# Kernel tuning notes

Measured on AMD Instinct MI355X. Metric: run time of the kernel, lower is better.

Reference implementation:

```python
import jax, jax.numpy as jnp
import numpy as np

U, SI, TI = 100000, 50000, 40000
D = 64
B = 8192
NNZ_S, NNZ_T = 3_200_000, 2_560_000
P_DROP = 0.2


def setup_inputs() -> dict:
    key = jax.random.key(0)
    ks = iter(jax.random.split(key, 32))
    nxt = lambda: next(ks)
    emb = lambda n: (jax.random.normal(nxt(), (n, D), jnp.float32) * 0.1)
    keep = lambda n: jax.random.bernoulli(nxt(), 1.0 - P_DROP, (n,)).astype(jnp.float32) / (1.0 - P_DROP)
    inp = {}
    inp['user'] = jax.random.randint(nxt(), (B,), 0, U, jnp.int32)
    inp['source_pos_item'] = jax.random.randint(nxt(), (B,), 0, SI, jnp.int32)
    inp['source_neg_item'] = jax.random.randint(nxt(), (B,), 0, SI, jnp.int32)
    inp['target_pos_item'] = jax.random.randint(nxt(), (B,), 0, TI, jnp.int32)
    inp['target_neg_item'] = jax.random.randint(nxt(), (B,), 0, TI, jnp.int32)
    inp['mask_s'] = jax.random.bernoulli(nxt(), 0.5, (B,))
    inp['mask_t'] = jax.random.bernoulli(nxt(), 0.5, (B,))
    inp['su_int'] = emb(U); inp['si_int'] = emb(SI)
    inp['tu_int'] = emb(U); inp['ti_int'] = emb(TI)
    inp['su_pop'] = emb(U); inp['si_pop'] = emb(SI)
    inp['tu_pop'] = emb(U); inp['ti_pop'] = emb(TI)
    Ns, Nt = U + SI, U + TI
    inp['s_rows'] = jax.random.randint(nxt(), (NNZ_S,), 0, Ns, jnp.int32)
    inp['s_cols'] = jax.random.randint(nxt(), (NNZ_S,), 0, Ns, jnp.int32)
    inp['s_vals'] = jax.random.uniform(nxt(), (NNZ_S,), jnp.float32, 0.0, 0.02)
    inp['t_rows'] = jax.random.randint(nxt(), (NNZ_T,), 0, Nt, jnp.int32)
    inp['t_cols'] = jax.random.randint(nxt(), (NNZ_T,), 0, Nt, jnp.int32)
    inp['t_vals'] = jax.random.uniform(nxt(), (NNZ_T,), jnp.float32, 0.0, 0.02)
    inp['drop_s_int'] = keep(NNZ_S); inp['drop_t_int'] = keep(NNZ_T)
    inp['drop_s_pop'] = keep(NNZ_S); inp['drop_t_pop'] = keep(NNZ_T)
    return inp


def _lightgcn(emb, rows, cols, vals, n_users):
    # 1-layer LightGCN: out = mean([e0, A @ e0]) ; A given as COO (rows, cols, vals)
    agg = jax.ops.segment_sum(vals[:, None] * emb[cols], rows, num_segments=emb.shape[0])
    out = 0.5 * (emb + agg)
    return out[:n_users], out[n_users:]


def _bpr(p, n):
    return -jnp.mean(jax.nn.log_sigmoid(p - n))


def _mask_bpr(p, n, m):
    return -jnp.mean(m.astype(p.dtype) * jax.nn.log_sigmoid(p - n))


def _masked_l1(a, b, idx):
    # L1Loss(mean) over rows selected by unique(idx); membership mask avoids jnp.unique
    m = jnp.zeros((a.shape[0],), bool).at[idx].set(True)
    cnt = jnp.maximum(m.sum(), 1).astype(a.dtype)
    return jnp.sum(jnp.abs(a - b) * m[:, None]) / (cnt * a.shape[1])


def reference(user, source_pos_item, source_neg_item, target_pos_item, target_neg_item,
              mask_s, mask_t,
              su_int, si_int, tu_int, ti_int, su_pop, si_pop, tu_pop, ti_pop,
              s_rows, s_cols, s_vals, t_rows, t_cols, t_vals,
              drop_s_int, drop_t_int, drop_s_pop, drop_t_pop):
    # int factor
    us_i, is_i = _lightgcn(jnp.concatenate([su_int, si_int]), s_rows, s_cols, s_vals * drop_s_int, U)
    ut_i, it_i = _lightgcn(jnp.concatenate([tu_int, ti_int]), t_rows, t_cols, t_vals * drop_t_int, U)
    # pop factor
    us_p, is_p = _lightgcn(jnp.concatenate([su_pop, si_pop]), s_rows, s_cols, s_vals * drop_s_pop, U)
    ut_p, it_p = _lightgcn(jnp.concatenate([tu_pop, ti_pop]), t_rows, t_cols, t_vals * drop_t_pop, U)

    dot = lambda ue, ie, u, i: jnp.sum(ue[u] * ie[i], axis=1)
    sp_i = dot(us_i, is_i, user, source_pos_item); sn_i = dot(us_i, is_i, user, source_neg_item)
    sp_p = dot(us_p, is_p, user, source_pos_item); sn_p = dot(us_p, is_p, user, source_neg_item)
    tp_i = dot(ut_i, it_i, user, target_pos_item); tn_i = dot(ut_i, it_i, user, target_neg_item)
    tp_p = dot(ut_p, it_p, user, target_pos_item); tn_p = dot(ut_p, it_p, user, target_neg_item)

    loss_int_s = _mask_bpr(sp_i, sn_i, mask_s)
    loss_pop_s = _mask_bpr(sn_p, sp_p, mask_s) + _mask_bpr(sp_p, sn_p, ~mask_s)
    loss_int_t = _mask_bpr(tp_i, tn_i, mask_t)
    loss_pop_t = _mask_bpr(tn_p, tp_p, mask_t) + _mask_bpr(tp_p, tn_p, ~mask_t)
    loss_total_s = _bpr(sp_i + sp_p, sn_i + sn_p)
    loss_total_t = _bpr(tp_i + tp_p, tn_i + tn_p)

    item_all_s = jnp.concatenate([source_pos_item, source_neg_item])
    item_all_t = jnp.concatenate([target_pos_item, target_neg_item])
    dis_loss = (_masked_l1(su_int, su_pop, user) + _masked_l1(si_int, si_pop, item_all_s)
                + _masked_l1(tu_int, tu_pop, user) + _masked_l1(ti_int, ti_pop, item_all_t))

    loss = (loss_total_s + loss_total_t
            + 0.1 * (loss_int_s + loss_int_t)
            + 0.1 * (loss_pop_s + loss_pop_t)
            - 0.01 * dis_loss)
    return loss
```

## Files before the change

kernel.cpp:

```cpp
#include <hip/hip_runtime.h>
#include <math.h>

constexpr int U_N = 100000;
constexpr int SI_N = 50000;
constexpr int TI_N = 40000;
constexpr int D = 64;
constexpr int B = 8192;
constexpr int NS = U_N + SI_N;
constexpr int NT = U_N + TI_N;
constexpr int SLOTS = 3 * B;
constexpr int CAP = 48;
constexpr int OVCAP = 4096;
constexpr int NROWS_ALL = U_N + SI_N + TI_N;
constexpr int NCHUNK = (NROWS_ALL + 63) / 64;
constexpr int DOTS_BLOCKS = B / 4;
constexpr int L1_BLOCKS = 768;

__device__ __forceinline__ float wave_sum(float x) {
#pragma unroll
  for (int m = 32; m; m >>= 1) x += __shfl_xor(x, m, 64);
  return x;
}

__device__ __forceinline__ float softplus_f(float z) {
  return fmaxf(z, 0.f) + log1pf(expf(-fabsf(z)));
}

__global__ __launch_bounds__(256) void k_init(
    const int* __restrict__ user, const int* __restrict__ spos, const int* __restrict__ sneg,
    const int* __restrict__ tpos, const int* __restrict__ tneg,
    int* __restrict__ map_s, int* __restrict__ map_t,
    const unsigned char* __restrict__ m, int* __restrict__ det) {
  if (blockIdx.x < 96) {
    int t = blockIdx.x * blockDim.x + threadIdx.x;
    if (t < B) {
      int u = user[t];
      map_s[u] = t;
      map_t[u] = t;
    } else if (t < 2 * B) {
      int b = t - B;
      map_s[U_N + spos[b]] = t;
      map_t[U_N + tpos[b]] = t;
    } else {
      int b = t - 2 * B;
      map_s[U_N + sneg[b]] = t;
      map_t[U_N + tneg[b]] = t;
    }
    return;
  }
  int t = threadIdx.x;
  int cb = 0, cc = 0;
  for (int i = t; i < B; i += 256) {
    unsigned char v = m[i];
    if ((i & 3) && v) cb++;
    if (v > 1) cc++;
  }
#pragma unroll
  for (int off = 32; off; off >>= 1) {
    cb += __shfl_xor(cb, off, 64);
    cc += __shfl_xor(cc, off, 64);
  }
  __shared__ int sb[4], sc[4];
  if ((t & 63) == 0) { sb[t >> 6] = cb; sc[t >> 6] = cc; }
  __syncthreads();
  if (t == 0) {
    det[0] = sb[0] + sb[1] + sb[2] + sb[3];
    det[1] = sc[0] + sc[1] + sc[2] + sc[3];
  }
}

__device__ __forceinline__ void emit_edge(
    int slot, unsigned packed, float vp,
    int* __restrict__ cnt, int2* __restrict__ bucket,
    int* __restrict__ ovcnt, int4* __restrict__ ov) {
  int pos = atomicAdd(&cnt[slot], 1);
  if (pos < CAP) {
    bucket[(size_t)slot * CAP + pos] = make_int2((int)packed, __float_as_int(vp));
  } else {
    int o = atomicAdd(ovcnt, 1);
    if (o < OVCAP) {
      ov[o] = make_int4(slot, (int)packed, __float_as_int(vp), 0);
    }
  }
}

__global__ __launch_bounds__(256) void k_compact4(
    const int* __restrict__ s_rows, const int* __restrict__ s_cols,
    const float* __restrict__ s_vals,
    const float* __restrict__ dsi, const float* __restrict__ dsp,
    const int* __restrict__ t_rows, const int* __restrict__ t_cols,
    const float* __restrict__ t_vals,
    const float* __restrict__ dti, const float* __restrict__ dtp,
    const int* __restrict__ map_s, const int* __restrict__ map_t,
    int* __restrict__ cnt_s, int* __restrict__ cnt_t,
    int2* __restrict__ bucket_s, int2* __restrict__ bucket_t,
    int* __restrict__ ovcnt_s, int* __restrict__ ovcnt_t,
    int4* __restrict__ ov_s, int4* __restrict__ ov_t,
    int nnz_s, int nnz_t, int sblocks) {
  const int* rows;
  const int* cols;
  const float* vals;
  const float* di;
  const float* dp;
  const int* map;
  int* cnt;
  int2* bucket;
  int* ovcnt;
  int4* ov;
  int nnz;
  int blk = blockIdx.x;
  if (blk < sblocks) {
    rows = s_rows; cols = s_cols; vals = s_vals; di = dsi; dp = dsp;
    map = map_s; cnt = cnt_s; bucket = bucket_s; ovcnt = ovcnt_s; ov = ov_s;
    nnz = nnz_s;
  } else {
    blk -= sblocks;
    rows = t_rows; cols = t_cols; vals = t_vals; di = dti; dp = dtp;
    map = map_t; cnt = cnt_t; bucket = bucket_t; ovcnt = ovcnt_t; ov = ov_t;
    nnz = nnz_t;
  }
  int base = (blk * 256 + (int)threadIdx.x) * 4;
  if (base + 4 <= nnz) {
    int4 r4 = *(const int4*)(rows + base);
    int4 c4 = *(const int4*)(cols + base);
    float4 v4 = *(const float4*)(vals + base);
    float4 di4 = *(const float4*)(di + base);
    float4 dp4 = *(const float4*)(dp + base);
    int s0 = map[r4.x];
    int s1 = map[r4.y];
    int s2 = map[r4.z];
    int s3 = map[r4.w];
    unsigned b0 = (di4.x != 0.f ? 0x40000000u : 0u) | (dp4.x != 0.f ? 0x80000000u : 0u);
    unsigned b1 = (di4.y != 0.f ? 0x40000000u : 0u) | (dp4.y != 0.f ? 0x80000000u : 0u);
    unsigned b2 = (di4.z != 0.f ? 0x40000000u : 0u) | (dp4.z != 0.f ? 0x80000000u : 0u);
    unsigned b3 = (di4.w != 0.f ? 0x40000000u : 0u) | (dp4.w != 0.f ? 0x80000000u : 0u);
    if (s0 >= 0 && b0) emit_edge(s0, (unsigned)c4.x | b0, v4.x * fmaxf(di4.x, dp4.x), cnt, bucket, ovcnt, ov);
    if (s1 >= 0 && b1) emit_edge(s1, (unsigned)c4.y | b1, v4.y * fmaxf(di4.y, dp4.y), cnt, bucket, ovcnt, ov);
    if (s2 >= 0 && b2) emit_edge(s2, (unsigned)c4.z | b2, v4.z * fmaxf(di4.z, dp4.z), cnt, bucket, ovcnt, ov);
    if (s3 >= 0 && b3) emit_edge(s3, (unsigned)c4.w | b3, v4.w * fmaxf(di4.w, dp4.w), cnt, bucket, ovcnt, ov);
  } else {
    for (int e = base; e < nnz; ++e) {
      int slot = map[rows[e]];
      if (slot < 0) continue;
      unsigned bb = (di[e] != 0.f ? 0x40000000u : 0u) | (dp[e] != 0.f ? 0x80000000u : 0u);
      if (!bb) continue;
      emit_edge(slot, (unsigned)cols[e] | bb, vals[e] * fmaxf(di[e], dp[e]), cnt, bucket, ovcnt, ov);
    }
  }
}

__device__ __forceinline__ void accum_slot(
    int s, int lane,
    const int* __restrict__ cnt, const int2* __restrict__ bucket,
    const int* __restrict__ ovcnt, const int4* __restrict__ ov,
    const float* __restrict__ eu_i, const float* __restrict__ ei_i,
    const float* __restrict__ eu_p, const float* __restrict__ ei_p,
    float* __restrict__ aggA, float* __restrict__ aggB) {
  int li = min(lane, CAP - 1);
  int2 pl = bucket[(size_t)s * CAP + li];
  int m = min(cnt[s], CAP);
  int g = lane >> 4, sub = lane & 15;
  int c = 0;
  float wi = 0.f, wp = 0.f;
  if (lane < m) {
    unsigned packed = (unsigned)pl.x;
    float vp = __int_as_float(pl.y);
    c = (int)(packed & 0x3FFFFFFFu);
    wi = (packed & 0x40000000u) ? vp : 0.f;
    wp = (packed & 0x80000000u) ? vp : 0.f;
  }
  float aIx = 0, aIy = 0, aIz = 0, aIw = 0;
  float aPx = 0, aPy = 0, aPz = 0, aPw = 0;
  for (int k = 0; k < m; k += 16) {
    int i0 = k + g, i1 = k + 4 + g, i2 = k + 8 + g, i3 = k + 12 + g;
    int c0 = __shfl(c, i0, 64), c1 = __shfl(c, i1, 64);
    int c2 = __shfl(c, i2, 64), c3 = __shfl(c, i3, 64);
    float wi0 = __shfl(wi, i0, 64), wi1 = __shfl(wi, i1, 64);
    float wi2 = __shfl(wi, i2, 64), wi3 = __shfl(wi, i3, 64);
    float wp0 = __shfl(wp, i0, 64), wp1 = __shfl(wp, i1, 64);
    float wp2 = __shfl(wp, i2, 64), wp3 = __shfl(wp, i3, 64);
    const float* bi0 = (c0 < U_N) ? (eu_i + (size_t)c0 * D) : (ei_i + (size_t)(c0 - U_N) * D);
    const float* bi1 = (c1 < U_N) ? (eu_i + (size_t)c1 * D) : (ei_i + (size_t)(c1 - U_N) * D);
    const float* bi2 = (c2 < U_N) ? (eu_i + (size_t)c2 * D) : (ei_i + (size_t)(c2 - U_N) * D);
    const float* bi3 = (c3 < U_N) ? (eu_i + (size_t)c3 * D) : (ei_i + (size_t)(c3 - U_N) * D);
    const float* bp0 = (c0 < U_N) ? (eu_p + (size_t)c0 * D) : (ei_p + (size_t)(c0 - U_N) * D);
    const float* bp1 = (c1 < U_N) ? (eu_p + (size_t)c1 * D) : (ei_p + (size_t)(c1 - U_N) * D);
    const float* bp2 = (c2 < U_N) ? (eu_p + (size_t)c2 * D) : (ei_p + (size_t)(c2 - U_N) * D);
    const float* bp3 = (c3 < U_N) ? (eu_p + (size_t)c3 * D) : (ei_p + (size_t)(c3 - U_N) * D);
    float4 vI0 = *(const float4*)(bi0 + 4 * sub);
    float4 vI1 = *(const float4*)(bi1 + 4 * sub);
    float4 vI2 = *(const float4*)(bi2 + 4 * sub);
    float4 vI3 = *(const float4*)(bi3 + 4 * sub);
    float4 vP0 = *(const float4*)(bp0 + 4 * sub);
    float4 vP1 = *(const float4*)(bp1 + 4 * sub);
    float4 vP2 = *(const float4*)(bp2 + 4 * sub);
    float4 vP3 = *(const float4*)(bp3 + 4 * sub);
    aIx = fmaf(wi0, vI0.x, aIx); aIy = fmaf(wi0, vI0.y, aIy);
    aIz = fmaf(wi0, vI0.z, aIz); aIw = fmaf(wi0, vI0.w, aIw);
    aIx = fmaf(wi1, vI1.x, aIx); aIy = fmaf(wi1, vI1.y, aIy);
    aIz = fmaf(wi1, vI1.z, aIz); aIw = fmaf(wi1, vI1.w, aIw);
    aIx = fmaf(wi2, vI2.x, aIx); aIy = fmaf(wi2, vI2.y, aIy);
    aIz = fmaf(wi2, vI2.z, aIz); aIw = fmaf(wi2, vI2.w, aIw);
    aIx = fmaf(wi3, vI3.x, aIx); aIy = fmaf(wi3, vI3.y, aIy);
    aIz = fmaf(wi3, vI3.z, aIz); aIw = fmaf(wi3, vI3.w, aIw);
    aPx = fmaf(wp0, vP0.x, aPx); aPy = fmaf(wp0, vP0.y, aPy);
    aPz = fmaf(wp0, vP0.z, aPz); aPw = fmaf(wp0, vP0.w, aPw);
    aPx = fmaf(wp1, vP1.x, aPx); aPy = fmaf(wp1, vP1.y, aPy);
    aPz = fmaf(wp1, vP1.z, aPz); aPw = fmaf(wp1, vP1.w, aPw);
    aPx = fmaf(wp2, vP2.x, aPx); aPy = fmaf(wp2, vP2.y, aPy);
    aPz = fmaf(wp2, vP2.z, aPz); aPw = fmaf(wp2, vP2.w, aPw);
    aPx = fmaf(wp3, vP3.x, aPx); aPy = fmaf(wp3, vP3.y, aPy);
    aPz = fmaf(wp3, vP3.z, aPz); aPw = fmaf(wp3, vP3.w, aPw);
  }
#define XRED(x) x += __shfl_xor(x, 16, 64); x += __shfl_xor(x, 32, 64);
  XRED(aIx) XRED(aIy) XRED(aIz) XRED(aIw)
  XRED(aPx) XRED(aPy) XRED(aPz) XRED(aPw)
#undef XRED
  int nov = min(*ovcnt, OVCAP);
  for (int i = 0; i < nov; ++i) {
    int4 q = ov[i];
    if (q.x == s) {
      unsigned packed = (unsigned)q.y;
      float vp = __int_as_float(q.z);
      int cc = (int)(packed & 0x3FFFFFFFu);
      float wwi = (packed & 0x40000000u) ? vp : 0.f;
      float wwp = (packed & 0x80000000u) ? vp : 0.f;
      const float* bi = (cc < U_N) ? (eu_i + (size_t)cc * D) : (ei_i + (size_t)(cc - U_N) * D);
      const float* bp = (cc < U_N) ? (eu_p + (size_t)cc * D) : (ei_p + (size_t)(cc - U_N) * D);
      if (lane < 16) {
        float4 vI = *(const float4*)(bi + 4 * sub);
        float4 vP = *(const float4*)(bp + 4 * sub);
        aIx = fmaf(wwi, vI.x, aIx); aIy = fmaf(wwi, vI.y, aIy);
        aIz = fmaf(wwi, vI.z, aIz); aIw = fmaf(wwi, vI.w, aIw);
        aPx = fmaf(wwp, vP.x, aPx); aPy = fmaf(wwp, vP.y, aPy);
        aPz = fmaf(wwp, vP.z, aPz); aPw = fmaf(wwp, vP.w, aPw);
      }
    }
  }
  if (lane < 16) {
    *(float4*)(aggA + (size_t)s * D + 4 * sub) = make_float4(aIx, aIy, aIz, aIw);
    *(float4*)(aggB + (size_t)s * D + 4 * sub) = make_float4(aPx, aPy, aPz, aPw);
  }
}

__global__ __launch_bounds__(256) void k_accum_pair(
    const int* __restrict__ cnt_s, const int2* __restrict__ bucket_s,
    const int* __restrict__ ovcnt_s, const int4* __restrict__ ov_s,
    const int* __restrict__ cnt_t, const int2* __restrict__ bucket_t,
    const int* __restrict__ ovcnt_t, const int4* __restrict__ ov_t,
    const float* __restrict__ su_i, const float* __restrict__ si_i,
    const float* __restrict__ su_p, const float* __restrict__ si_p,
    const float* __restrict__ tu_i, const float* __restrict__ ti_i,
    const float* __restrict__ tu_p, const float* __restrict__ ti_p,
    float* __restrict__ aggSA, float* __restrict__ aggSB,
    float* __restrict__ aggTA, float* __restrict__ aggTB) {
  int lane = threadIdx.x & 63;
  int sg = (blockIdx.x * 256 + threadIdx.x) >> 6;
  if (sg >= 2 * SLOTS) return;
  if (sg < SLOTS) {
    accum_slot(sg, lane, cnt_s, bucket_s, ovcnt_s, ov_s,
               su_i, si_i, su_p, si_p, aggSA, aggSB);
  } else {
    accum_slot(sg - SLOTS, lane, cnt_t, bucket_t, ovcnt_t, ov_t,
               tu_i, ti_i, tu_p, ti_p, aggTA, aggTB);
  }
}

__global__ __launch_bounds__(256) void k_tail(
    const int* __restrict__ user,
    const int* __restrict__ spos, const int* __restrict__ sneg,
    const int* __restrict__ tpos, const int* __restrict__ tneg,
    const unsigned char* __restrict__ ms8, const unsigned char* __restrict__ mt8,
    const int* __restrict__ det,
    const float* __restrict__ su_i, const float* __restrict__ si_i,
    const float* __restrict__ su_p, const float* __restrict__ si_p,
    const float* __restrict__ tu_i, const float* __restrict__ ti_i,
    const float* __restrict__ tu_p, const float* __restrict__ ti_p,
    const int* __restrict__ map_s, const int* __restrict__ map_t,
    const float* __restrict__ aggSA, const float* __restrict__ aggSB,
    const float* __restrict__ aggTA, const float* __restrict__ aggTB,
    float* __restrict__ dots_part, float* __restrict__ l1_part) {
  int lane = threadIdx.x & 63;
  if (blockIdx.x < DOTS_BLOCKS) {
    int b = (blockIdx.x * blockDim.x + threadIdx.x) >> 6;
    float contrib = 0.f;
    {
      int u = user[b];
      int ps = spos[b], ns = sneg[b], pt = tpos[b], nt = tneg[b];
      int sus = map_s[u], sps = map_s[U_N + ps], sns = map_s[U_N + ns];
      int sut = map_t[u], spt = map_t[U_N + pt], snt = map_t[U_N + nt];
      float oui = su_i[(size_t)u * D + lane] + aggSA[(size_t)sus * D + lane];
      float oup = su_p[(size_t)u * D + lane] + aggSB[(size_t)sus * D + lane];
      float opi = si_i[(size_t)ps * D + lane] + aggSA[(size_t)sps * D + lane];
      float opp = si_p[(size_t)ps * D + lane] + aggSB[(size_t)sps * D + lane];
      float oni = si_i[(size_t)ns * D + lane] + aggSA[(size_t)sns * D + lane];
      float onp = si_p[(size_t)ns * D + lane] + aggSB[(size_t)sns * D + lane];
      float spi = 0.25f * wave_sum(oui * opi);
      float sni = 0.25f * wave_sum(oui * oni);
      float spp = 0.25f * wave_sum(oup * opp);
      float snp = 0.25f * wave_sum(oup * onp);
      float tui = tu_i[(size_t)u * D + lane] + aggTA[(size_t)sut * D + lane];
      float tup = tu_p[(size_t)u * D + lane] + aggTB[(size_t)sut * D + lane];
      float tpi_ = ti_i[(size_t)pt * D + lane] + aggTA[(size_t)spt * D + lane];
      float tpp_ = ti_p[(size_t)pt * D + lane] + aggTB[(size_t)spt * D + lane];
      float tni_ = ti_i[(size_t)nt * D + lane] + aggTA[(size_t)snt * D + lane];
      float tnp_ = ti_p[(size_t)nt * D + lane] + aggTB[(size_t)snt * D + lane];
      float tpi = 0.25f * wave_sum(tui * tpi_);
      float tni = 0.25f * wave_sum(tui * tni_);
      float tpp = 0.25f * wave_sum(tup * tpp_);
      float tnp = 0.25f * wave_sum(tup * tnp_);
      int db = det[0], dc = det[1];
      float ms, mt;
      if (dc > 100) {
        ms = (((const float*)ms8)[b] != 0.f) ? 1.f : 0.f;
        mt = (((const float*)mt8)[b] != 0.f) ? 1.f : 0.f;
      } else if (db > 100) {
        ms = ms8[b] ? 1.f : 0.f;
        mt = mt8[b] ? 1.f : 0.f;
      } else {
        ms = ((const int*)ms8)[b] ? 1.f : 0.f;
        mt = ((const int*)mt8)[b] ? 1.f : 0.f;
      }
      float l_int_s = ms * softplus_f(sni - spi);
      float l_pop_s = ms * softplus_f(spp - snp) + (1.f - ms) * softplus_f(snp - spp);
      float l_tot_s = softplus_f((sni + snp) - (spi + spp));
      float l_int_t = mt * softplus_f(tni - tpi);
      float l_pop_t = mt * softplus_f(tpp - tnp) + (1.f - mt) * softplus_f(tnp - tpp);
      float l_tot_t = softplus_f((tni + tnp) - (tpi + tpp));
      contrib = (l_tot_s + l_tot_t + 0.1f * (l_int_s + l_int_t) +
                 0.1f * (l_pop_s + l_pop_t)) * (1.f / (float)B);
    }
    __shared__ float wsum_[4];
    if (lane == 0) wsum_[threadIdx.x >> 6] = contrib;
    __syncthreads();
    if (threadIdx.x == 0) {
      dots_part[blockIdx.x] = wsum_[0] + wsum_[1] + wsum_[2] + wsum_[3];
    }
    return;
  }
  int blk = blockIdx.x - DOTS_BLOCKS;
  int wave = (blk * blockDim.x + threadIdx.x) >> 6;
  int nwaves = (L1_BLOCKS * 256) >> 6;
  float a1 = 0.f, a2 = 0.f, a3 = 0.f, a4 = 0.f;
  float c5 = 0.f, c6 = 0.f, c7 = 0.f;
  for (int ch = wave; ch < NCHUNK; ch += nwaves) {
    int r0 = ch * 64;
    int r = r0 + lane;
    int flag = -1;
    if (r < NROWS_ALL) flag = (r < NS) ? map_s[r] : map_t[r - SI_N];
    bool valid = flag >= 0;
    unsigned long long m0 = __ballot(valid && r < U_N);
    unsigned long long m1 = __ballot(valid && r >= U_N && r < NS);
    unsigned long long m2 = __ballot(valid && r >= NS);
    if (lane == 0) {
      c5 += (float)__popcll(m0);
      c6 += (float)__popcll(m1);
      c7 += (float)__popcll(m2);
    }
    unsigned long long mm = m0 | m1 | m2;
    while (mm) {
      int bit = __ffsll((unsigned long long)mm) - 1;
      mm &= mm - 1;
      int rr = r0 + bit;
      if (rr < U_N) {
        size_t o = (size_t)rr * D + lane;
        a1 += fabsf(su_i[o] - su_p[o]);
        a3 += fabsf(tu_i[o] - tu_p[o]);
      } else if (rr < NS) {
        size_t o = (size_t)(rr - U_N) * D + lane;
        a2 += fabsf(si_i[o] - si_p[o]);
      } else {
        size_t o = (size_t)(rr - NS) * D + lane;
        a4 += fabsf(ti_i[o] - ti_p[o]);
      }
    }
  }
  a1 = wave_sum(a1);
  a2 = wave_sum(a2);
  a3 = wave_sum(a3);
  a4 = wave_sum(a4);
  __shared__ float sb[4][8];
  if (lane == 0) {
    int w = threadIdx.x >> 6;
    sb[w][0] = a1; sb[w][1] = a2; sb[w][2] = a3; sb[w][3] = a4;
    sb[w][4] = c5; sb[w][5] = c6; sb[w][6] = c7;
  }
  __syncthreads();
  int t = threadIdx.x;
  if (t < 7) {
    l1_part[t * L1_BLOCKS + blk] = sb[0][t] + sb[1][t] + sb[2][t] + sb[3][t];
  }
}

__global__ __launch_bounds__(256) void k_finish(
    const float* __restrict__ dots_part, const float* __restrict__ l1_part,
    float* __restrict__ out) {
  int t = threadIdx.x, lane = t & 63, w = t >> 6;
  float a0 = 0.f;
  for (int i = t; i < DOTS_BLOCKS; i += 256) a0 += dots_part[i];
  float q[7];
#pragma unroll
  for (int j = 0; j < 7; ++j) {
    float s = 0.f;
    for (int i = t; i < L1_BLOCKS; i += 256) s += l1_part[j * L1_BLOCKS + i];
    q[j] = s;
  }
  a0 = wave_sum(a0);
#pragma unroll
  for (int j = 0; j < 7; ++j) q[j] = wave_sum(q[j]);
  __shared__ float red[4][8];
  if (lane == 0) {
    red[w][0] = a0;
#pragma unroll
    for (int j = 0; j < 7; ++j) red[w][1 + j] = q[j];
  }
  __syncthreads();
  if (t == 0) {
    float v[8];
#pragma unroll
    for (int j = 0; j < 8; ++j)
      v[j] = red[0][j] + red[1][j] + red[2][j] + red[3][j];
    float n1 = v[1], n2 = v[2], n3 = v[3], n4 = v[4];
    float cu = fmaxf(v[5], 1.f);
    float cs = fmaxf(v[6], 1.f);
    float ct = fmaxf(v[7], 1.f);
    float dis = (n1 + n3) / (cu * (float)D) + n2 / (cs * (float)D) +
                n4 / (ct * (float)D);
    out[0] = v[0] - 0.01f * dis;
  }
}

extern "C" void kernel_launch(void* const* d_in, const int* in_sizes, int n_in,
                              void* d_out, int out_size, void* d_ws, size_t ws_size,
                              hipStream_t stream) {
  const int* user = (const int*)d_in[0];
  const int* spos = (const int*)d_in[1];
  const int* sneg = (const int*)d_in[2];
  const int* tpos = (const int*)d_in[3];
  const int* tneg = (const int*)d_in[4];
  const unsigned char* mask_s = (const unsigned char*)d_in[5];
  const unsigned char* mask_t = (const unsigned char*)d_in[6];
  const float* su_int = (const float*)d_in[7];
  const float* si_int = (const float*)d_in[8];
  const float* tu_int = (const float*)d_in[9];
  const float* ti_int = (const float*)d_in[10];
  const float* su_pop = (const float*)d_in[11];
  const float* si_pop = (const float*)d_in[12];
  const float* tu_pop = (const float*)d_in[13];
  const float* ti_pop = (const float*)d_in[14];
  const int* s_rows = (const int*)d_in[15];
  const int* s_cols = (const int*)d_in[16];
  const float* s_vals = (const float*)d_in[17];
  const int* t_rows = (const int*)d_in[18];
  const int* t_cols = (const int*)d_in[19];
  const float* t_vals = (const float*)d_in[20];
  const float* drop_s_int = (const float*)d_in[21];
  const float* drop_t_int = (const float*)d_in[22];
  const float* drop_s_pop = (const float*)d_in[23];
  const float* drop_t_pop = (const float*)d_in[24];
  const int nnz_s = in_sizes[15];
  const int nnz_t = in_sizes[18];

  int4* ov_s = (int4*)d_ws;
  int4* ov_t = ov_s + OVCAP;
  int2* bucket_s = (int2*)(ov_t + OVCAP);
  int2* bucket_t = bucket_s + (size_t)SLOTS * CAP;
  float* aggSA = (float*)(bucket_t + (size_t)SLOTS * CAP);
  float* aggSB = aggSA + (size_t)SLOTS * D;
  float* aggTA = aggSB + (size_t)SLOTS * D;
  float* aggTB = aggTA + (size_t)SLOTS * D;
  float* dots_part = aggTB + (size_t)SLOTS * D;
  float* l1_part = dots_part + DOTS_BLOCKS;
  int* det = (int*)(l1_part + 7 * L1_BLOCKS);
  int* ovcnt_s = det + 2;
  int* ovcnt_t = ovcnt_s + 1;
  int* cnt_s = ovcnt_t + 1;
  int* cnt_t = cnt_s + SLOTS;
  int* map_s = cnt_t + SLOTS;
  int* map_t = map_s + NS;

  hipMemsetAsync(det, 0, (size_t)(2 + 2 + 2 * SLOTS) * sizeof(int), stream);
  hipMemsetAsync(map_s, 0xFF, (size_t)(NS + NT) * sizeof(int), stream);

  k_init<<<97, 256, 0, stream>>>(user, spos, sneg, tpos, tneg, map_s, map_t, mask_s, det);

  int sblocks = (nnz_s + 1023) / 1024;
  int tblocks = (nnz_t + 1023) / 1024;
  k_compact4<<<sblocks + tblocks, 256, 0, stream>>>(
      s_rows, s_cols, s_vals, drop_s_int, drop_s_pop,
      t_rows, t_cols, t_vals, drop_t_int, drop_t_pop,
      map_s, map_t, cnt_s, cnt_t, bucket_s, bucket_t,
      ovcnt_s, ovcnt_t, ov_s, ov_t, nnz_s, nnz_t, sblocks);

  k_accum_pair<<<2 * SLOTS / 4, 256, 0, stream>>>(
      cnt_s, bucket_s, ovcnt_s, ov_s, cnt_t, bucket_t, ovcnt_t, ov_t,
      su_int, si_int, su_pop, si_pop, tu_int, ti_int, tu_pop, ti_pop,
      aggSA, aggSB, aggTA, aggTB);

  k_tail<<<DOTS_BLOCKS + L1_BLOCKS, 256, 0, stream>>>(
      user, spos, sneg, tpos, tneg, mask_s, mask_t, det,
      su_int, si_int, su_pop, si_pop, tu_int, ti_int, tu_pop, ti_pop,
      map_s, map_t, aggSA, aggSB, aggTA, aggTB,
      dots_part, l1_part);

  k_finish<<<1, 256, 0, stream>>>(dots_part, l1_part, (float*)d_out);
}
```

Baseline: 400.5 us.

## Partition edge bucket counters per XCD to avoid cross-die atomic contention

Edge compaction now writes into eight separate per-XCD bucket and counter arrays, selected by blockIdx modulo 8, each holding 12 entries per slot. The idea is that atomics on each counter stay within one die's L2 instead of bouncing across XCDs. The accumulate step reads all eight counters per slot, forms prefix offsets, and gathers entries from the matching partition. This adds more counter reads, a more complex gather, and a larger memset. Overflow risk rises because each partition holds only 12 entries, so skew past that falls into the shared linear overflow scan.

```diff
diff --git a/kernel.cpp b/kernel.cpp
--- a/kernel.cpp
+++ b/kernel.cpp
@@ -9,7 +9,8 @@
 constexpr int NS = U_N + SI_N;
 constexpr int NT = U_N + TI_N;
 constexpr int SLOTS = 3 * B;
-constexpr int CAP = 48;
+constexpr int NXCD = 8;
+constexpr int CAP_X = 12;
 constexpr int OVCAP = 4096;
 constexpr int NROWS_ALL = U_N + SI_N + TI_N;
 constexpr int NCHUNK = (NROWS_ALL + 63) / 64;
@@ -74,8 +75,8 @@
     int* __restrict__ cnt, int2* __restrict__ bucket,
     int* __restrict__ ovcnt, int4* __restrict__ ov) {
   int pos = atomicAdd(&cnt[slot], 1);
-  if (pos < CAP) {
-    bucket[(size_t)slot * CAP + pos] = make_int2((int)packed, __float_as_int(vp));
+  if (pos < CAP_X) {
+    bucket[(size_t)slot * CAP_X + pos] = make_int2((int)packed, __float_as_int(vp));
   } else {
     int o = atomicAdd(ovcnt, 1);
     if (o < OVCAP) {
@@ -119,6 +120,9 @@
     map = map_t; cnt = cnt_t; bucket = bucket_t; ovcnt = ovcnt_t; ov = ov_t;
     nnz = nnz_t;
   }
+  int p = (int)(blockIdx.x & (NXCD - 1));
+  cnt += (size_t)p * SLOTS;
+  bucket += (size_t)p * SLOTS * CAP_X;
   int base = (blk * 256 + (int)threadIdx.x) * 4;
   if (base + 4 <= nnz) {
     int4 r4 = *(const int4*)(rows + base);
@@ -156,61 +160,80 @@
     const float* __restrict__ eu_i, const float* __restrict__ ei_i,
     const float* __restrict__ eu_p, const float* __restrict__ ei_p,
     float* __restrict__ aggA, float* __restrict__ aggB) {
-  int li = min(lane, CAP - 1);
-  int2 pl = bucket[(size_t)s * CAP + li];
-  int m = min(cnt[s], CAP);
+  int c0 = min(cnt[0 * SLOTS + s], CAP_X);
+  int c1 = min(cnt[1 * SLOTS + s], CAP_X);
+  int c2 = min(cnt[2 * SLOTS + s], CAP_X);
+  int c3 = min(cnt[3 * SLOTS + s], CAP_X);
+  int c4 = min(cnt[4 * SLOTS + s], CAP_X);
+  int c5 = min(cnt[5 * SLOTS + s], CAP_X);
+  int c6 = min(cnt[6 * SLOTS + s], CAP_X);
+  int c7 = min(cnt[7 * SLOTS + s], CAP_X);
+  int p1 = c0, p2 = p1 + c1, p3 = p2 + c2, p4 = p3 + c3;
+  int p5 = p4 + c4, p6 = p5 + c5, p7 = p6 + c6;
+  int m = p7 + c7;
   int g = lane >> 4, sub = lane & 15;
-  int c = 0;
-  float wi = 0.f, wp = 0.f;
-  if (lane < m) {
-    unsigned packed = (unsigned)pl.x;
-    float vp = __int_as_float(pl.y);
-    c = (int)(packed & 0x3FFFFFFFu);
-    wi = (packed & 0x40000000u) ? vp : 0.f;
-    wp = (packed & 0x80000000u) ? vp : 0.f;
-  }
   float aIx = 0, aIy = 0, aIz = 0, aIw = 0;
   float aPx = 0, aPy = 0, aPz = 0, aPw = 0;
-  for (int k = 0; k < m; k += 16) {
-    int i0 = k + g, i1 = k + 4 + g, i2 = k + 8 + g, i3 = k + 12 + g;
-    int c0 = __shfl(c, i0, 64), c1 = __shfl(c, i1, 64);
-    int c2 = __shfl(c, i2, 64), c3 = __shfl(c, i3, 64);
-    float wi0 = __shfl(wi, i0, 64), wi1 = __shfl(wi, i1, 64);
-    float wi2 = __shfl(wi, i2, 64), wi3 = __shfl(wi, i3, 64);
-    float wp0 = __shfl(wp, i0, 64), wp1 = __shfl(wp, i1, 64);
-    float wp2 = __shfl(wp, i2, 64), wp3 = __shfl(wp, i3, 64);
-    const float* bi0 = (c0 < U_N) ? (eu_i + (size_t)c0 * D) : (ei_i + (size_t)(c0 - U_N) * D);
-    const float* bi1 = (c1 < U_N) ? (eu_i + (size_t)c1 * D) : (ei_i + (size_t)(c1 - U_N) * D);
-    const float* bi2 = (c2 < U_N) ? (eu_i + (size_t)c2 * D) : (ei_i + (size_t)(c2 - U_N) * D);
-    const float* bi3 = (c3 < U_N) ? (eu_i + (size_t)c3 * D) : (ei_i + (size_t)(c3 - U_N) * D);
-    const float* bp0 = (c0 < U_N) ? (eu_p + (size_t)c0 * D) : (ei_p + (size_t)(c0 - U_N) * D);
-    const float* bp1 = (c1 < U_N) ? (eu_p + (size_t)c1 * D) : (ei_p + (size_t)(c1 - U_N) * D);
-    const float* bp2 = (c2 < U_N) ? (eu_p + (size_t)c2 * D) : (ei_p + (size_t)(c2 - U_N) * D);
-    const float* bp3 = (c3 < U_N) ? (eu_p + (size_t)c3 * D) : (ei_p + (size_t)(c3 - U_N) * D);
-    float4 vI0 = *(const float4*)(bi0 + 4 * sub);
-    float4 vI1 = *(const float4*)(bi1 + 4 * sub);
-    float4 vI2 = *(const float4*)(bi2 + 4 * sub);
-    float4 vI3 = *(const float4*)(bi3 + 4 * sub);
-    float4 vP0 = *(const float4*)(bp0 + 4 * sub);
-    float4 vP1 = *(const float4*)(bp1 + 4 * sub);
-    float4 vP2 = *(const float4*)(bp2 + 4 * sub);
-    float4 vP3 = *(const float4*)(bp3 + 4 * sub);
-    aIx = fmaf(wi0, vI0.x, aIx); aIy = fmaf(wi0, vI0.y, aIy);
-    aIz = fmaf(wi0, vI0.z, aIz); aIw = fmaf(wi0, vI0.w, aIw);
-    aIx = fmaf(wi1, vI1.x, aIx); aIy = fmaf(wi1, vI1.y, aIy);
-    aIz = fmaf(wi1, vI1.z, aIz); aIw = fmaf(wi1, vI1.w, aIw);
-    aIx = fmaf(wi2, vI2.x, aIx); aIy = fmaf(wi2, vI2.y, aIy);
-    aIz = fmaf(wi2, vI2.z, aIz); aIw = fmaf(wi2, vI2.w, aIw);
-    aIx = fmaf(wi3, vI3.x, aIx); aIy = fmaf(wi3, vI3.y, aIy);
-    aIz = fmaf(wi3, vI3.z, aIz); aIw = fmaf(wi3, vI3.w, aIw);
-    aPx = fmaf(wp0, vP0.x, aPx); aPy = fmaf(wp0, vP0.y, aPy);
-    aPz = fmaf(wp0, vP0.z, aPz); aPw = fmaf(wp0, vP0.w, aPw);
-    aPx = fmaf(wp1, vP1.x, aPx); aPy = fmaf(wp1, vP1.y, aPy);
-    aPz = fmaf(wp1, vP1.z, aPz); aPw = fmaf(wp1, vP1.w, aPw);
-    aPx = fmaf(wp2, vP2.x, aPx); aPy = fmaf(wp2, vP2.y, aPy);
-    aPz = fmaf(wp2, vP2.z, aPz); aPw = fmaf(wp2, vP2.w, aPw);
-    aPx = fmaf(wp3, vP3.x, aPx); aPy = fmaf(wp3, vP3.y, aPy);
-    aPz = fmaf(wp3, vP3.z, aPz); aPw = fmaf(wp3, vP3.w, aPw);
+  for (int bb = 0; bb < m; bb += 64) {
+    int l = bb + lane;
+    int c = 0;
+    float wi = 0.f, wp = 0.f;
+    if (l < m) {
+      int x = (l >= p1) + (l >= p2) + (l >= p3) + (l >= p4) +
+              (l >= p5) + (l >= p6) + (l >= p7);
+      int pre = (x >= 1 ? c0 : 0) + (x >= 2 ? c1 : 0) + (x >= 3 ? c2 : 0) +
+                (x >= 4 ? c3 : 0) + (x >= 5 ? c4 : 0) + (x >= 6 ? c5 : 0) +
+                (x >= 7 ? c6 : 0);
+      int j = l - pre;
+      int2 pl = bucket[((size_t)x * SLOTS + s) * CAP_X + j];
+      unsigned packed = (unsigned)pl.x;
+      float vp = __int_as_float(pl.y);
+      c = (int)(packed & 0x3FFFFFFFu);
+      wi = (packed & 0x40000000u) ? vp : 0.f;
+      wp = (packed & 0x80000000u) ? vp : 0.f;
+    }
+    int mb = min(m - bb, 64);
+    for (int k = 0; k < mb; k += 16) {
+      int i0 = k + g, i1 = k + 4 + g, i2 = k + 8 + g, i3 = k + 12 + g;
+      int cc0 = __shfl(c, i0, 64), cc1 = __shfl(c, i1, 64);
+      int cc2 = __shfl(c, i2, 64), cc3 = __shfl(c, i3, 64);
+      float wi0 = __shfl(wi, i0, 64), wi1 = __shfl(wi, i1, 64);
+      float wi2 = __shfl(wi, i2, 64), wi3 = __shfl(wi, i3, 64);
+      float wp0 = __shfl(wp, i0, 64), wp1 = __shfl(wp, i1, 64);
+      float wp2 = __shfl(wp, i2, 64), wp3 = __shfl(wp, i3, 64);
+      const float* bi0 = (cc0 < U_N) ? (eu_i + (size_t)cc0 * D) : (ei_i + (size_t)(cc0 - U_N) * D);
+      const float* bi1 = (cc1 < U_N) ? (eu_i + (size_t)cc1 * D) : (ei_i + (size_t)(cc1 - U_N) * D);
+      const float* bi2 = (cc2 < U_N) ? (eu_i + (size_t)cc2 * D) : (ei_i + (size_t)(cc2 - U_N) * D);
+      const float* bi3 = (cc3 < U_N) ? (eu_i + (size_t)cc3 * D) : (ei_i + (size_t)(cc3 - U_N) * D);
+      const float* bp0 = (cc0 < U_N) ? (eu_p + (size_t)cc0 * D) : (ei_p + (size_t)(cc0 - U_N) * D);
+      const float* bp1 = (cc1 < U_N) ? (eu_p + (size_t)cc1 * D) : (ei_p + (size_t)(cc1 - U_N) * D);
+      const float* bp2 = (cc2 < U_N) ? (eu_p + (size_t)cc2 * D) : (ei_p + (size_t)(cc2 - U_N) * D);
+      const float* bp3 = (cc3 < U_N) ? (eu_p + (size_t)cc3 * D) : (ei_p + (size_t)(cc3 - U_N) * D);
+      float4 vI0 = *(const float4*)(bi0 + 4 * sub);
+      float4 vI1 = *(const float4*)(bi1 + 4 * sub);
+      float4 vI2 = *(const float4*)(bi2 + 4 * sub);
+      float4 vI3 = *(const float4*)(bi3 + 4 * sub);
+      float4 vP0 = *(const float4*)(bp0 + 4 * sub);
+      float4 vP1 = *(const float4*)(bp1 + 4 * sub);
+      float4 vP2 = *(const float4*)(bp2 + 4 * sub);
+      float4 vP3 = *(const float4*)(bp3 + 4 * sub);
+      aIx = fmaf(wi0, vI0.x, aIx); aIy = fmaf(wi0, vI0.y, aIy);
+      aIz = fmaf(wi0, vI0.z, aIz); aIw = fmaf(wi0, vI0.w, aIw);
+      aIx = fmaf(wi1, vI1.x, aIx); aIy = fmaf(wi1, vI1.y, aIy);
+      aIz = fmaf(wi1, vI1.z, aIz); aIw = fmaf(wi1, vI1.w, aIw);
+      aIx = fmaf(wi2, vI2.x, aIx); aIy = fmaf(wi2, vI2.y, aIy);
+      aIz = fmaf(wi2, vI2.z, aIz); aIw = fmaf(wi2, vI2.w, aIw);
+      aIx = fmaf(wi3, vI3.x, aIx); aIy = fmaf(wi3, vI3.y, aIy);
+      aIz = fmaf(wi3, vI3.z, aIz); aIw = fmaf(wi3, vI3.w, aIw);
+      aPx = fmaf(wp0, vP0.x, aPx); aPy = fmaf(wp0, vP0.y, aPy);
+      aPz = fmaf(wp0, vP0.z, aPz); aPw = fmaf(wp0, vP0.w, aPw);
+      aPx = fmaf(wp1, vP1.x, aPx); aPy = fmaf(wp1, vP1.y, aPy);
+      aPz = fmaf(wp1, vP1.z, aPz); aPw = fmaf(wp1, vP1.w, aPw);
+      aPx = fmaf(wp2, vP2.x, aPx); aPy = fmaf(wp2, vP2.y, aPy);
+      aPz = fmaf(wp2, vP2.z, aPz); aPw = fmaf(wp2, vP2.w, aPw);
+      aPx = fmaf(wp3, vP3.x, aPx); aPy = fmaf(wp3, vP3.y, aPy);
+      aPz = fmaf(wp3, vP3.z, aPz); aPw = fmaf(wp3, vP3.w, aPw);
+    }
   }
 #define XRED(x) x += __shfl_xor(x, 16, 64); x += __shfl_xor(x, 32, 64);
   XRED(aIx) XRED(aIy) XRED(aIz) XRED(aIw)
@@ -464,8 +487,8 @@
   int4* ov_s = (int4*)d_ws;
   int4* ov_t = ov_s + OVCAP;
   int2* bucket_s = (int2*)(ov_t + OVCAP);
-  int2* bucket_t = bucket_s + (size_t)SLOTS * CAP;
-  float* aggSA = (float*)(bucket_t + (size_t)SLOTS * CAP);
+  int2* bucket_t = bucket_s + (size_t)NXCD * SLOTS * CAP_X;
+  float* aggSA = (float*)(bucket_t + (size_t)NXCD * SLOTS * CAP_X);
   float* aggSB = aggSA + (size_t)SLOTS * D;
   float* aggTA = aggSB + (size_t)SLOTS * D;
   float* aggTB = aggTA + (size_t)SLOTS * D;
@@ -475,11 +498,11 @@
   int* ovcnt_s = det + 2;
   int* ovcnt_t = ovcnt_s + 1;
   int* cnt_s = ovcnt_t + 1;
-  int* cnt_t = cnt_s + SLOTS;
-  int* map_s = cnt_t + SLOTS;
+  int* cnt_t = cnt_s + (size_t)NXCD * SLOTS;
+  int* map_s = cnt_t + (size_t)NXCD * SLOTS;
   int* map_t = map_s + NS;
 
-  hipMemsetAsync(det, 0, (size_t)(2 + 2 + 2 * SLOTS) * sizeof(int), stream);
+  hipMemsetAsync(det, 0, (size_t)(2 + 2 + 2 * NXCD * SLOTS) * sizeof(int), stream);
   hipMemsetAsync(map_s, 0xFF, (size_t)(NS + NT) * sizeof(int), stream);
 
   k_init<<<97, 256, 0, stream>>>(user, spos, sneg, tpos, tneg, map_s, map_t, mask_s, det);
```

After: 417.9 us. 1.04x slower.

## Partition edge-bucket counters per XCD with a shared secondary spill bucket

Applied to the files above, without the earlier changes.

Each of the 8 XCD partitions (chosen from blockIdx mod 8) now gets its own counter array and an 8-entry sub-bucket per slot. The intent is to keep atomics within one XCD's L2 and avoid cross-die contention on shared counters. Overflow goes to a 16-entry shared secondary bucket and then to the existing global overflow list. The accumulate kernel always runs four fully unrolled 16-edge passes over the 64 partitioned entries, plus one more pass when the secondary bucket is in use. This trades more memset traffic and fixed gather work per slot for cheaper atomics.

```diff
diff --git a/kernel.cpp b/kernel.cpp
--- a/kernel.cpp
+++ b/kernel.cpp
@@ -9,7 +9,10 @@
 constexpr int NS = U_N + SI_N;
 constexpr int NT = U_N + TI_N;
 constexpr int SLOTS = 3 * B;
-constexpr int CAP = 48;
+constexpr int NXCD = 8;
+constexpr int CAP_X = 8;
+constexpr int SLOT_POS = NXCD * CAP_X;
+constexpr int CAP2 = 16;
 constexpr int OVCAP = 4096;
 constexpr int NROWS_ALL = U_N + SI_N + TI_N;
 constexpr int NCHUNK = (NROWS_ALL + 63) / 64;
@@ -70,16 +73,23 @@
 }
 
 __device__ __forceinline__ void emit_edge(
-    int slot, unsigned packed, float vp,
+    int slot, int p, unsigned packed, float vp,
     int* __restrict__ cnt, int2* __restrict__ bucket,
+    int* __restrict__ cnt2, int2* __restrict__ bucket2,
     int* __restrict__ ovcnt, int4* __restrict__ ov) {
   int pos = atomicAdd(&cnt[slot], 1);
-  if (pos < CAP) {
-    bucket[(size_t)slot * CAP + pos] = make_int2((int)packed, __float_as_int(vp));
+  if (pos < CAP_X) {
+    bucket[(size_t)slot * SLOT_POS + p * CAP_X + pos] =
+        make_int2((int)packed, __float_as_int(vp));
   } else {
-    int o = atomicAdd(ovcnt, 1);
-    if (o < OVCAP) {
-      ov[o] = make_int4(slot, (int)packed, __float_as_int(vp), 0);
+    int q = atomicAdd(&cnt2[slot], 1);
+    if (q < CAP2) {
+      bucket2[(size_t)slot * CAP2 + q] = make_int2((int)packed, __float_as_int(vp));
+    } else {
+      int o = atomicAdd(ovcnt, 1);
+      if (o < OVCAP) {
+        ov[o] = make_int4(slot, (int)packed, __float_as_int(vp), 0);
+      }
     }
   }
 }
@@ -94,6 +104,8 @@
     const int* __restrict__ map_s, const int* __restrict__ map_t,
     int* __restrict__ cnt_s, int* __restrict__ cnt_t,
     int2* __restrict__ bucket_s, int2* __restrict__ bucket_t,
+    int* __restrict__ cnt2_s, int* __restrict__ cnt2_t,
+    int2* __restrict__ bucket2_s, int2* __restrict__ bucket2_t,
     int* __restrict__ ovcnt_s, int* __restrict__ ovcnt_t,
     int4* __restrict__ ov_s, int4* __restrict__ ov_t,
     int nnz_s, int nnz_t, int sblocks) {
@@ -105,20 +117,24 @@
   const int* map;
   int* cnt;
   int2* bucket;
+  int* cnt2;
+  int2* bucket2;
   int* ovcnt;
   int4* ov;
   int nnz;
   int blk = blockIdx.x;
   if (blk < sblocks) {
     rows = s_rows; cols = s_cols; vals = s_vals; di = dsi; dp = dsp;
-    map = map_s; cnt = cnt_s; bucket = bucket_s; ovcnt = ovcnt_s; ov = ov_s;
-    nnz = nnz_s;
+    map = map_s; cnt = cnt_s; bucket = bucket_s; cnt2 = cnt2_s; bucket2 = bucket2_s;
+    ovcnt = ovcnt_s; ov = ov_s; nnz = nnz_s;
   } else {
     blk -= sblocks;
     rows = t_rows; cols = t_cols; vals = t_vals; di = dti; dp = dtp;
-    map = map_t; cnt = cnt_t; bucket = bucket_t; ovcnt = ovcnt_t; ov = ov_t;
-    nnz = nnz_t;
-  }
+    map = map_t; cnt = cnt_t; bucket = bucket_t; cnt2 = cnt2_t; bucket2 = bucket2_t;
+    ovcnt = ovcnt_t; ov = ov_t; nnz = nnz_t;
+  }
+  int p = (int)(blockIdx.x & (NXCD - 1));
+  cnt += (size_t)p * SLOTS;
   int base = (blk * 256 + (int)threadIdx.x) * 4;
   if (base + 4 <= nnz) {
     int4 r4 = *(const int4*)(rows + base);
@@ -134,35 +150,79 @@
     unsigned b1 = (di4.y != 0.f ? 0x40000000u : 0u) | (dp4.y != 0.f ? 0x80000000u : 0u);
     unsigned b2 = (di4.z != 0.f ? 0x40000000u : 0u) | (dp4.z != 0.f ? 0x80000000u : 0u);
     unsigned b3 = (di4.w != 0.f ? 0x40000000u : 0u) | (dp4.w != 0.f ? 0x80000000u : 0u);
-    if (s0 >= 0 && b0) emit_edge(s0, (unsigned)c4.x | b0, v4.x * fmaxf(di4.x, dp4.x), cnt, bucket, ovcnt, ov);
-    if (s1 >= 0 && b1) emit_edge(s1, (unsigned)c4.y | b1, v4.y * fmaxf(di4.y, dp4.y), cnt, bucket, ovcnt, ov);
-    if (s2 >= 0 && b2) emit_edge(s2, (unsigned)c4.z | b2, v4.z * fmaxf(di4.z, dp4.z), cnt, bucket, ovcnt, ov);
-    if (s3 >= 0 && b3) emit_edge(s3, (unsigned)c4.w | b3, v4.w * fmaxf(di4.w, dp4.w), cnt, bucket, ovcnt, ov);
+    if (s0 >= 0 && b0) emit_edge(s0, p, (unsigned)c4.x | b0, v4.x * fmaxf(di4.x, dp4.x), cnt, bucket, cnt2, bucket2, ovcnt, ov);
+    if (s1 >= 0 && b1) emit_edge(s1, p, (unsigned)c4.y | b1, v4.y * fmaxf(di4.y, dp4.y), cnt, bucket, cnt2, bucket2, ovcnt, ov);
+    if (s2 >= 0 && b2) emit_edge(s2, p, (unsigned)c4.z | b2, v4.z * fmaxf(di4.z, dp4.z), cnt, bucket, cnt2, bucket2, ovcnt, ov);
+    if (s3 >= 0 && b3) emit_edge(s3, p, (unsigned)c4.w | b3, v4.w * fmaxf(di4.w, dp4.w), cnt, bucket, cnt2, bucket2, ovcnt, ov);
   } else {
     for (int e = base; e < nnz; ++e) {
       int slot = map[rows[e]];
       if (slot < 0) continue;
       unsigned bb = (di[e] != 0.f ? 0x40000000u : 0u) | (dp[e] != 0.f ? 0x80000000u : 0u);
       if (!bb) continue;
-      emit_edge(slot, (unsigned)cols[e] | bb, vals[e] * fmaxf(di[e], dp[e]), cnt, bucket, ovcnt, ov);
-    }
-  }
-}
+      emit_edge(slot, p, (unsigned)cols[e] | bb, vals[e] * fmaxf(di[e], dp[e]), cnt, bucket, cnt2, bucket2, ovcnt, ov);
+    }
+  }
+}
+
+#define MAC16(kk)                                                              \
+  {                                                                            \
+    int i0 = (kk) + g, i1 = (kk) + 4 + g, i2 = (kk) + 8 + g, i3 = (kk) + 12 + g; \
+    int cc0 = __shfl(c, i0, 64), cc1 = __shfl(c, i1, 64);                      \
+    int cc2 = __shfl(c, i2, 64), cc3 = __shfl(c, i3, 64);                      \
+    float wi0 = __shfl(wi, i0, 64), wi1 = __shfl(wi, i1, 64);                  \
+    float wi2 = __shfl(wi, i2, 64), wi3 = __shfl(wi, i3, 64);                  \
+    float wp0 = __shfl(wp, i0, 64), wp1 = __shfl(wp, i1, 64);                  \
+    float wp2 = __shfl(wp, i2, 64), wp3 = __shfl(wp, i3, 64);                  \
+    const float* bi0 = (cc0 < U_N) ? (eu_i + (size_t)cc0 * D) : (ei_i + (size_t)(cc0 - U_N) * D); \
+    const float* bi1 = (cc1 < U_N) ? (eu_i + (size_t)cc1 * D) : (ei_i + (size_t)(cc1 - U_N) * D); \
+    const float* bi2 = (cc2 < U_N) ? (eu_i + (size_t)cc2 * D) : (ei_i + (size_t)(cc2 - U_N) * D); \
+    const float* bi3 = (cc3 < U_N) ? (eu_i + (size_t)cc3 * D) : (ei_i + (size_t)(cc3 - U_N) * D); \
+    const float* bp0 = (cc0 < U_N) ? (eu_p + (size_t)cc0 * D) : (ei_p + (size_t)(cc0 - U_N) * D); \
+    const float* bp1 = (cc1 < U_N) ? (eu_p + (size_t)cc1 * D) : (ei_p + (size_t)(cc1 - U_N) * D); \
+    const float* bp2 = (cc2 < U_N) ? (eu_p + (size_t)cc2 * D) : (ei_p + (size_t)(cc2 - U_N) * D); \
+    const float* bp3 = (cc3 < U_N) ? (eu_p + (size_t)cc3 * D) : (ei_p + (size_t)(cc3 - U_N) * D); \
+    float4 vI0 = *(const float4*)(bi0 + 4 * sub);                              \
+    float4 vI1 = *(const float4*)(bi1 + 4 * sub);                              \
+    float4 vI2 = *(const float4*)(bi2 + 4 * sub);                              \
+    float4 vI3 = *(const float4*)(bi3 + 4 * sub);                              \
+    float4 vP0 = *(const float4*)(bp0 + 4 * sub);                              \
+    float4 vP1 = *(const float4*)(bp1 + 4 * sub);                              \
+    float4 vP2 = *(const float4*)(bp2 + 4 * sub);                              \
+    float4 vP3 = *(const float4*)(bp3 + 4 * sub);                              \
+    aIx = fmaf(wi0, vI0.x, aIx); aIy = fmaf(wi0, vI0.y, aIy);                  \
+    aIz = fmaf(wi0, vI0.z, aIz); aIw = fmaf(wi0, vI0.w, aIw);                  \
+    aIx = fmaf(wi1, vI1.x, aIx); aIy = fmaf(wi1, vI1.y, aIy);                  \
+    aIz = fmaf(wi1, vI1.z, aIz); aIw = fmaf(wi1, vI1.w, aIw);                  \
+    aIx = fmaf(wi2, vI2.x, aIx); aIy = fmaf(wi2, vI2.y, aIy);                  \
+    aIz = fmaf(wi2, vI2.z, aIz); aIw = fmaf(wi2, vI2.w, aIw);                  \
+    aIx = fmaf(wi3, vI3.x, aIx); aIy = fmaf(wi3, vI3.y, aIy);                  \
+    aIz = fmaf(wi3, vI3.z, aIz); aIw = fmaf(wi3, vI3.w, aIw);                  \
+    aPx = fmaf(wp0, vP0.x, aPx); aPy = fmaf(wp0, vP0.y, aPy);                  \
+    aPz = fmaf(wp0, vP0.z, aPz); aPw = fmaf(wp0, vP0.w, aPw);                  \
+    aPx = fmaf(wp1, vP1.x, aPx); aPy = fmaf(wp1, vP1.y, aPy);                  \
+    aPz = fmaf(wp1, vP1.z, aPz); aPw = fmaf(wp1, vP1.w, aPw);                  \
+    aPx = fmaf(wp2, vP2.x, aPx); aPy = fmaf(wp2, vP2.y, aPy);                  \
+    aPz = fmaf(wp2, vP2.z, aPz); aPw = fmaf(wp2, vP2.w, aPw);                  \
+    aPx = fmaf(wp3, vP3.x, aPx); aPy = fmaf(wp3, vP3.y, aPy);                  \
+    aPz = fmaf(wp3, vP3.z, aPz); aPw = fmaf(wp3, vP3.w, aPw);                  \
+  }
 
 __device__ __forceinline__ void accum_slot(
     int s, int lane,
     const int* __restrict__ cnt, const int2* __restrict__ bucket,
+    const int* __restrict__ cnt2, const int2* __restrict__ bucket2,
     const int* __restrict__ ovcnt, const int4* __restrict__ ov,
     const float* __restrict__ eu_i, const float* __restrict__ ei_i,
     const float* __restrict__ eu_p, const float* __restrict__ ei_p,
     float* __restrict__ aggA, float* __restrict__ aggB) {
-  int li = min(lane, CAP - 1);
-  int2 pl = bucket[(size_t)s * CAP + li];
-  int m = min(cnt[s], CAP);
+  int2 pl = bucket[(size_t)s * SLOT_POS + lane];
+  int cp = cnt[(lane >> 3) * SLOTS + s];
+  int c2 = cnt2[s];
   int g = lane >> 4, sub = lane & 15;
   int c = 0;
   float wi = 0.f, wp = 0.f;
-  if (lane < m) {
+  if ((lane & 7) < min(cp, CAP_X)) {
     unsigned packed = (unsigned)pl.x;
     float vp = __int_as_float(pl.y);
     c = (int)(packed & 0x3FFFFFFFu);
@@ -171,46 +231,19 @@
   }
   float aIx = 0, aIy = 0, aIz = 0, aIw = 0;
   float aPx = 0, aPy = 0, aPz = 0, aPw = 0;
-  for (int k = 0; k < m; k += 16) {
-    int i0 = k + g, i1 = k + 4 + g, i2 = k + 8 + g, i3 = k + 12 + g;
-    int c0 = __shfl(c, i0, 64), c1 = __shfl(c, i1, 64);
-    int c2 = __shfl(c, i2, 64), c3 = __shfl(c, i3, 64);
-    float wi0 = __shfl(wi, i0, 64), wi1 = __shfl(wi, i1, 64);
-    float wi2 = __shfl(wi, i2, 64), wi3 = __shfl(wi, i3, 64);
-    float wp0 = __shfl(wp, i0, 64), wp1 = __shfl(wp, i1, 64);
-    float wp2 = __shfl(wp, i2, 64), wp3 = __shfl(wp, i3, 64);
-    const float* bi0 = (c0 < U_N) ? (eu_i + (size_t)c0 * D) : (ei_i + (size_t)(c0 - U_N) * D);
-    const float* bi1 = (c1 < U_N) ? (eu_i + (size_t)c1 * D) : (ei_i + (size_t)(c1 - U_N) * D);
-    const float* bi2 = (c2 < U_N) ? (eu_i + (size_t)c2 * D) : (ei_i + (size_t)(c2 - U_N) * D);
-    const float* bi3 = (c3 < U_N) ? (eu_i + (size_t)c3 * D) : (ei_i + (size_t)(c3 - U_N) * D);
-    const float* bp0 = (c0 < U_N) ? (eu_p + (size_t)c0 * D) : (ei_p + (size_t)(c0 - U_N) * D);
-    const float* bp1 = (c1 < U_N) ? (eu_p + (size_t)c1 * D) : (ei_p + (size_t)(c1 - U_N) * D);
-    const float* bp2 = (c2 < U_N) ? (eu_p + (size_t)c2 * D) : (ei_p + (size_t)(c2 - U_N) * D);
-    const float* bp3 = (c3 < U_N) ? (eu_p + (size_t)c3 * D) : (ei_p + (size_t)(c3 - U_N) * D);
-    float4 vI0 = *(const float4*)(bi0 + 4 * sub);
-    float4 vI1 = *(const float4*)(bi1 + 4 * sub);
-    float4 vI2 = *(const float4*)(bi2 + 4 * sub);
-    float4 vI3 = *(const float4*)(bi3 + 4 * sub);
-    float4 vP0 = *(const float4*)(bp0 + 4 * sub);
-    float4 vP1 = *(const float4*)(bp1 + 4 * sub);
-    float4 vP2 = *(const float4*)(bp2 + 4 * sub);
-    float4 vP3 = *(const float4*)(bp3 + 4 * sub);
-    aIx = fmaf(wi0, vI0.x, aIx); aIy = fmaf(wi0, vI0.y, aIy);
-    aIz = fmaf(wi0, vI0.z, aIz); aIw = fmaf(wi0, vI0.w, aIw);
-    aIx = fmaf(wi1, vI1.x, aIx); aIy = fmaf(wi1, vI1.y, aIy);
-    aIz = fmaf(wi1, vI1.z, aIz); aIw = fmaf(wi1, vI1.w, aIw);
-    aIx = fmaf(wi2, vI2.x, aIx); aIy = fmaf(wi2, vI2.y, aIy);
-    aIz = fmaf(wi2, vI2.z, aIz); aIw = fmaf(wi2, vI2.w, aIw);
-    aIx = fmaf(wi3, vI3.x, aIx); aIy = fmaf(wi3, vI3.y, aIy);
-    aIz = fmaf(wi3, vI3.z, aIz); aIw = fmaf(wi3, vI3.w, aIw);
-    aPx = fmaf(wp0, vP0.x, aPx); aPy = fmaf(wp0, vP0.y, aPy);
-    aPz = fmaf(wp0, vP0.z, aPz); aPw = fmaf(wp0, vP0.w, aPw);
-    aPx = fmaf(wp1, vP1.x, aPx); aPy = fmaf(wp1, vP1.y, aPy);
-    aPz = fmaf(wp1, vP1.z, aPz); aPw = fmaf(wp1, vP1.w, aPw);
-    aPx = fmaf(wp2, vP2.x, aPx); aPy = fmaf(wp2, vP2.y, aPy);
-    aPz = fmaf(wp2, vP2.z, aPz); aPw = fmaf(wp2, vP2.w, aPw);
-    aPx = fmaf(wp3, vP3.x, aPx); aPy = fmaf(wp3, vP3.y, aPy);
-    aPz = fmaf(wp3, vP3.z, aPz); aPw = fmaf(wp3, vP3.w, aPw);
+  MAC16(0) MAC16(16) MAC16(32) MAC16(48)
+  if (c2 > 0) {
+    int m2 = min(c2, CAP2);
+    c = 0; wi = 0.f; wp = 0.f;
+    if (lane < m2) {
+      int2 q = bucket2[(size_t)s * CAP2 + lane];
+      unsigned packed = (unsigned)q.x;
+      float vp = __int_as_float(q.y);
+      c = (int)(packed & 0x3FFFFFFFu);
+      wi = (packed & 0x40000000u) ? vp : 0.f;
+      wp = (packed & 0x80000000u) ? vp : 0.f;
+    }
+    MAC16(0)
   }
 #define XRED(x) x += __shfl_xor(x, 16, 64); x += __shfl_xor(x, 32, 64);
   XRED(aIx) XRED(aIy) XRED(aIz) XRED(aIw)
@@ -245,8 +278,10 @@
 
 __global__ __launch_bounds__(256) void k_accum_pair(
     const int* __restrict__ cnt_s, const int2* __restrict__ bucket_s,
+    const int* __restrict__ cnt2_s, const int2* __restrict__ bucket2_s,
     const int* __restrict__ ovcnt_s, const int4* __restrict__ ov_s,
     const int* __restrict__ cnt_t, const int2* __restrict__ bucket_t,
+    const int* __restrict__ cnt2_t, const int2* __restrict__ bucket2_t,
     const int* __restrict__ ovcnt_t, const int4* __restrict__ ov_t,
     const float* __restrict__ su_i, const float* __restrict__ si_i,
     const float* __restrict__ su_p, const float* __restrict__ si_p,
@@ -258,10 +293,10 @@
   int sg = (blockIdx.x * 256 + threadIdx.x) >> 6;
   if (sg >= 2 * SLOTS) return;
   if (sg < SLOTS) {
-    accum_slot(sg, lane, cnt_s, bucket_s, ovcnt_s, ov_s,
+    accum_slot(sg, lane, cnt_s, bucket_s, cnt2_s, bucket2_s, ovcnt_s, ov_s,
                su_i, si_i, su_p, si_p, aggSA, aggSB);
   } else {
-    accum_slot(sg - SLOTS, lane, cnt_t, bucket_t, ovcnt_t, ov_t,
+    accum_slot(sg - SLOTS, lane, cnt_t, bucket_t, cnt2_t, bucket2_t, ovcnt_t, ov_t,
                tu_i, ti_i, tu_p, ti_p, aggTA, aggTB);
   }
 }
@@ -464,8 +499,10 @@
   int4* ov_s = (int4*)d_ws;
   int4* ov_t = ov_s + OVCAP;
   int2* bucket_s = (int2*)(ov_t + OVCAP);
-  int2* bucket_t = bucket_s + (size_t)SLOTS * CAP;
-  float* aggSA = (float*)(bucket_t + (size_t)SLOTS * CAP);
+  int2* bucket_t = bucket_s + (size_t)SLOTS * SLOT_POS;
+  int2* bucket2_s = bucket_t + (size_t)SLOTS * SLOT_POS;
+  int2* bucket2_t = bucket2_s + (size_t)SLOTS * CAP2;
+  float* aggSA = (float*)(bucket2_t + (size_t)SLOTS * CAP2);
   float* aggSB = aggSA + (size_t)SLOTS * D;
   float* aggTA = aggSB + (size_t)SLOTS * D;
   float* aggTB = aggTA + (size_t)SLOTS * D;
@@ -475,11 +512,14 @@
   int* ovcnt_s = det + 2;
   int* ovcnt_t = ovcnt_s + 1;
   int* cnt_s = ovcnt_t + 1;
-  int* cnt_t = cnt_s + SLOTS;
-  int* map_s = cnt_t + SLOTS;
+  int* cnt_t = cnt_s + (size_t)NXCD * SLOTS;
+  int* cnt2_s = cnt_t + (size_t)NXCD * SLOTS;
+  int* cnt2_t = cnt2_s + SLOTS;
+  int* map_s = cnt2_t + SLOTS;
   int* map_t = map_s + NS;
 
-  hipMemsetAsync(det, 0, (size_t)(2 + 2 + 2 * SLOTS) * sizeof(int), stream);
+  hipMemsetAsync(det, 0,
+                 (size_t)(2 + 2 + 2 * NXCD * SLOTS + 2 * SLOTS) * sizeof(int), stream);
   hipMemsetAsync(map_s, 0xFF, (size_t)(NS + NT) * sizeof(int), stream);
 
   k_init<<<97, 256, 0, stream>>>(user, spos, sneg, tpos, tneg, map_s, map_t, mask_s, det);
@@ -490,10 +530,12 @@
       s_rows, s_cols, s_vals, drop_s_int, drop_s_pop,
       t_rows, t_cols, t_vals, drop_t_int, drop_t_pop,
       map_s, map_t, cnt_s, cnt_t, bucket_s, bucket_t,
+      cnt2_s, cnt2_t, bucket2_s, bucket2_t,
       ovcnt_s, ovcnt_t, ov_s, ov_t, nnz_s, nnz_t, sblocks);
 
   k_accum_pair<<<2 * SLOTS / 4, 256, 0, stream>>>(
-      cnt_s, bucket_s, ovcnt_s, ov_s, cnt_t, bucket_t, ovcnt_t, ov_t,
+      cnt_s, bucket_s, cnt2_s, bucket2_s, ovcnt_s, ov_s,
+      cnt_t, bucket_t, cnt2_t, bucket2_t, ovcnt_t, ov_t,
       su_int, si_int, su_pop, si_pop, tu_int, ti_int, tu_pop, ti_pop,
       aggSA, aggSB, aggTA, aggTB);
 
```

Result: slower. 422.3 us (+5.4%).
